# Optimization experiments

Measured on AMD Instinct MI355X. Metric: run time of the kernel, lower is better.

## Reference

```python
import jax, jax.numpy as jnp
import numpy as np
import math

FACIL_RATE = 2.0
FIRE_THRESH = 0.85
MAX_GATE = 8.0
N_BUF = 512
TOP_K_FRAC = 0.1
B, T, D = 4, 4096, 2048


def _gelu(x):
    c = math.sqrt(2.0 / math.pi)
    return 0.5 * x * (1.0 + jnp.tanh(c * (x + 0.044715 * x * x * x)))


def setup_inputs() -> dict:
    key = jax.random.key(0)
    k1, k2, k3 = jax.random.split(key, 3)
    x = jax.random.normal(k1, (B, T, D), dtype=jnp.float32)
    log_strength = jnp.asarray(0.0, dtype=jnp.float32)
    # Steady-state ring buffer: keys = normalized mean vectors, masks = top-k(|mean|) indicators
    means = jax.random.normal(k2, (N_BUF, D), dtype=jnp.float32)
    buf_keys = means / jnp.linalg.norm(means, axis=-1, keepdims=True)
    top_k = max(1, int(D * TOP_K_FRAC))  # 204
    _, top_idx = jax.lax.top_k(jnp.abs(means), top_k)  # (N_BUF, top_k)
    buf_masks = jnp.zeros((N_BUF, D), dtype=jnp.float32).at[
        jnp.arange(N_BUF)[:, None], top_idx].set(1.0)
    facil = 1.0 + 3.0 * jax.random.uniform(k3, (N_BUF,), dtype=jnp.float32)
    valid_mask = jnp.ones((N_BUF,), dtype=bool)
    return {"x": x, "log_strength": log_strength, "buf_keys": buf_keys,
            "buf_masks": buf_masks, "facil": facil, "valid_mask": valid_mask}


def reference(x, log_strength, buf_keys, buf_masks, facil, valid_mask):
    # Steady-state (pass1_complete) path of GELU277.forward
    y = _gelu(x)  # (B, T, D)
    # m_curr = y.detach().flatten(0,1).mean(0)  -> stop_gradient as in torch no_grad
    m_curr = jax.lax.stop_gradient(y).reshape(-1, y.shape[-1]).mean(0)  # (D,)
    q = m_curr / jnp.linalg.norm(m_curr)
    sims = buf_keys @ q                      # (N_BUF,) cosine similarities
    sims = jnp.where(valid_mask, sims, -1.0)
    nearest = jnp.argmax(sims)
    sim_max = sims[nearest]
    # facil[nearest] *= FACIL_RATE if fired, then read (.item() in torch -> constant)
    f = jax.lax.stop_gradient(facil[nearest]) * jnp.where(sim_max > FIRE_THRESH, FACIL_RATE, 1.0)
    # strength.item() in torch -> no grad through log_strength
    strength = jax.lax.stop_gradient(jnp.clip(jnp.exp(log_strength), 0.01, 5.0))
    k_amp = jnp.minimum(1.0 + strength * (f - 1.0), MAX_GATE)
    topk_mask = jax.lax.stop_gradient(buf_masks[nearest])  # (D,)
    gate = 1.0 + (k_amp - 1.0) * topk_mask
    return y * gate[None, None, :]
```

## Files before the change

### kernel.cpp

```cpp
#include <hip/hip_runtime.h>
#include <math.h>

#define DCOLS 2048
#define NROWS 16384
#define NBUF  512

typedef float v4f __attribute__((ext_vector_type(4)));

__device__ __forceinline__ float gelu_f(float x) {
    const float c = 0.7978845608028654f;
    float u = c * (x + 0.044715f * x * x * x);
    float e = __expf(2.0f * u);
    float t = 1.0f - 2.0f / (1.0f + e);
    return 0.5f * x * (1.0f + t);
}

__global__ __launch_bounds__(512) void k_colsum_part(const float* __restrict__ x,
                                                     float* __restrict__ part) {
    int t = threadIdx.x;
    int col = t * 4;
    float a0 = 0.f, a1 = 0.f, a2 = 0.f, a3 = 0.f;
    for (int r = blockIdx.x; r < NROWS; r += gridDim.x) {
        float4 v = *reinterpret_cast<const float4*>(x + (size_t)r * DCOLS + col);
        a0 += gelu_f(v.x); a1 += gelu_f(v.y); a2 += gelu_f(v.z); a3 += gelu_f(v.w);
    }
    float4 st; st.x = a0; st.y = a1; st.z = a2; st.w = a3;
    *reinterpret_cast<float4*>(part + (size_t)blockIdx.x * DCOLS + col) = st;
}

__global__ __launch_bounds__(512) void k_colsum_atomic(const float* __restrict__ x,
                                                       float* __restrict__ colsum) {
    int t = threadIdx.x;
    int col = t * 4;
    float a0 = 0.f, a1 = 0.f, a2 = 0.f, a3 = 0.f;
    for (int r = blockIdx.x; r < NROWS; r += gridDim.x) {
        float4 v = *reinterpret_cast<const float4*>(x + (size_t)r * DCOLS + col);
        a0 += gelu_f(v.x); a1 += gelu_f(v.y); a2 += gelu_f(v.z); a3 += gelu_f(v.w);
    }
    atomicAdd(&colsum[col + 0], a0);
    atomicAdd(&colsum[col + 1], a1);
    atomicAdd(&colsum[col + 2], a2);
    atomicAdd(&colsum[col + 3], a3);
}

__global__ __launch_bounds__(256) void k_colsum_reduce(const float* __restrict__ part,
                                                       float* __restrict__ colsum) {
    int col = blockIdx.x * 256 + threadIdx.x;
    int base = blockIdx.y * 64;
    float a = 0.f;
#pragma unroll 8
    for (int b = 0; b < 64; ++b)
        a += part[(size_t)(base + b) * DCOLS + col];
    atomicAdd(&colsum[col], a);
}

__global__ __launch_bounds__(256) void k_sims(const float* __restrict__ keys,
                                              const float* __restrict__ colsum,
                                              float* __restrict__ s) {
    __shared__ float wsum[4];
    int row = blockIdx.x;
    int t = threadIdx.x;
    const float* kr = keys + (size_t)row * DCOLS;
    int j = t * 8;
    float4 k0 = *reinterpret_cast<const float4*>(kr + j);
    float4 k1 = *reinterpret_cast<const float4*>(kr + j + 4);
    float4 c0 = *reinterpret_cast<const float4*>(colsum + j);
    float4 c1 = *reinterpret_cast<const float4*>(colsum + j + 4);
    float acc = k0.x * c0.x + k0.y * c0.y + k0.z * c0.z + k0.w * c0.w
              + k1.x * c1.x + k1.y * c1.y + k1.z * c1.z + k1.w * c1.w;
    for (int off = 32; off; off >>= 1) acc += __shfl_down(acc, off);
    if ((t & 63) == 0) wsum[t >> 6] = acc;
    __syncthreads();
    if (t == 0) s[row] = wsum[0] + wsum[1] + wsum[2] + wsum[3];
}

__global__ __launch_bounds__(256) void k_gate(const float* __restrict__ colsum,
                                              const float* __restrict__ s,
                                              const float* __restrict__ log_strength,
                                              const float* __restrict__ facil,
                                              const float* __restrict__ masks,
                                              float* __restrict__ gate) {
    __shared__ float red[256];
    __shared__ int   redi[256];
    int t = threadIdx.x;

    float n2 = 0.f;
    for (int j = t; j < DCOLS; j += 256) { float v = colsum[j]; n2 += v * v; }
    red[t] = n2; __syncthreads();
    for (int off = 128; off; off >>= 1) {
        if (t < off) red[t] += red[t + off];
        __syncthreads();
    }
    float norm = sqrtf(red[0]);
    __syncthreads();

    float best = -1e30f; int bi = 0x7fffffff;
    for (int j = t; j < NBUF; j += 256) {
        float v = s[j];
        if (v > best || (v == best && j < bi)) { best = v; bi = j; }
    }
    red[t] = best; redi[t] = bi; __syncthreads();
    for (int off = 128; off; off >>= 1) {
        if (t < off) {
            float ov = red[t + off]; int oi = redi[t + off];
            if (ov > red[t] || (ov == red[t] && oi < redi[t])) { red[t] = ov; redi[t] = oi; }
        }
        __syncthreads();
    }
    int nearest = redi[0];
    float sim_max = red[0] / norm;

    float strength = __expf(log_strength[0]);
    strength = fminf(fmaxf(strength, 0.01f), 5.0f);
    float f = facil[nearest] * (sim_max > 0.85f ? 2.0f : 1.0f);
    float k_amp = fminf(1.0f + strength * (f - 1.0f), 8.0f);

    const float* mrow = masks + (size_t)nearest * DCOLS;
    for (int j = t; j < DCOLS; j += 256)
        gate[j] = 1.0f + (k_amp - 1.0f) * mrow[j];
}

__global__ __launch_bounds__(256) void k_scale(const float* __restrict__ x,
                                               const float* __restrict__ gate,
                                               float* __restrict__ out) {
    int t = threadIdx.x;
    int col = t * 8;
    float4 g0 = *reinterpret_cast<const float4*>(gate + col);
    float4 g1 = *reinterpret_cast<const float4*>(gate + col + 4);
    for (int r = blockIdx.x; r < NROWS; r += gridDim.x) {
        size_t off = (size_t)r * DCOLS + col;
        float4 v0 = *reinterpret_cast<const float4*>(x + off);
        float4 v1 = *reinterpret_cast<const float4*>(x + off + 4);
        v4f o0, o1;
        o0.x = gelu_f(v0.x) * g0.x;
        o0.y = gelu_f(v0.y) * g0.y;
        o0.z = gelu_f(v0.z) * g0.z;
        o0.w = gelu_f(v0.w) * g0.w;
        o1.x = gelu_f(v1.x) * g1.x;
        o1.y = gelu_f(v1.y) * g1.y;
        o1.z = gelu_f(v1.z) * g1.z;
        o1.w = gelu_f(v1.w) * g1.w;
        __builtin_nontemporal_store(o0, reinterpret_cast<v4f*>(out + off));
        __builtin_nontemporal_store(o1, reinterpret_cast<v4f*>(out + off + 4));
    }
}

extern "C" void kernel_launch(void* const* d_in, const int* in_sizes, int n_in,
                              void* d_out, int out_size, void* d_ws, size_t ws_size,
                              hipStream_t stream) {
    const float* x            = (const float*)d_in[0];
    const float* log_strength = (const float*)d_in[1];
    const float* keys         = (const float*)d_in[2];
    const float* masks        = (const float*)d_in[3];
    const float* facil        = (const float*)d_in[4];
    float* out = (float*)d_out;
    float* ws  = (float*)d_ws;

    float* colsum = ws;
    float* s      = ws + 2048;
    float* gate   = ws + 2560;
    float* part   = ws + 4608;

    auto need = [](int nbp) {
        return (size_t)(4608 + (size_t)nbp * DCOLS) * sizeof(float);
    };

    int nbp = 0;
    if (ws_size >= need(1024)) nbp = 1024;
    else if (ws_size >= need(512)) nbp = 512;

    (void)hipMemsetAsync(colsum, 0, DCOLS * sizeof(float), stream);

    if (nbp) {
        k_colsum_part<<<nbp, 512, 0, stream>>>(x, part);
        dim3 rg(DCOLS / 256, nbp / 64);
        k_colsum_reduce<<<rg, 256, 0, stream>>>(part, colsum);
    } else {
        k_colsum_atomic<<<512, 512, 0, stream>>>(x, colsum);
    }
    k_sims<<<NBUF, 256, 0, stream>>>(keys, colsum, s);
    k_gate<<<1, 256, 0, stream>>>(colsum, s, log_strength, facil, masks, gate);
    k_scale<<<2048, 256, 0, stream>>>(x, gate, out);
}
```

Measured before the change: 95.41 us.

## Write GELU output in reduction pass and rescale only gated columns afterward

The first pass now writes GELU(x) straight to the output while it accumulates column sums, so the second pass no longer re-reads x or recomputes GELU. Instead a sparse pass reads back and rescales only the 8-column groups whose gate differs from 1. The similarity and gate kernels are merged through a last-block atomic counter, and the memset is folded into the first kernel, which removes launches. The risk is that about 57% of column groups hold a masked column, so the rescale pass may still touch most cache lines and add read-modify-write traffic.

```diff
diff --git a/kernel.cpp b/kernel.cpp
--- a/kernel.cpp
+++ b/kernel.cpp
@@ -15,32 +15,38 @@
     return 0.5f * x * (1.0f + t);
 }
 
-__global__ __launch_bounds__(512) void k_colsum_part(const float* __restrict__ x,
-                                                     float* __restrict__ part) {
+__global__ __launch_bounds__(512) void k_pass1(const float* __restrict__ x,
+                                               float* __restrict__ out,
+                                               float* __restrict__ part,
+                                               float* __restrict__ colsum,
+                                               int* __restrict__ counter,
+                                               int do_zero) {
     int t = threadIdx.x;
     int col = t * 4;
+    if (do_zero && blockIdx.x == 0) {
+        colsum[t] = 0.f; colsum[t + 512] = 0.f;
+        colsum[t + 1024] = 0.f; colsum[t + 1536] = 0.f;
+        if (t == 0) *counter = 0;
+    }
     float a0 = 0.f, a1 = 0.f, a2 = 0.f, a3 = 0.f;
+#pragma unroll 2
     for (int r = blockIdx.x; r < NROWS; r += gridDim.x) {
-        float4 v = *reinterpret_cast<const float4*>(x + (size_t)r * DCOLS + col);
-        a0 += gelu_f(v.x); a1 += gelu_f(v.y); a2 += gelu_f(v.z); a3 += gelu_f(v.w);
+        size_t off = (size_t)r * DCOLS + col;
+        v4f v = __builtin_nontemporal_load(reinterpret_cast<const v4f*>(x + off));
+        v4f o;
+        o.x = gelu_f(v.x); o.y = gelu_f(v.y); o.z = gelu_f(v.z); o.w = gelu_f(v.w);
+        a0 += o.x; a1 += o.y; a2 += o.z; a3 += o.w;
+        *reinterpret_cast<v4f*>(out + off) = o;
     }
-    float4 st; st.x = a0; st.y = a1; st.z = a2; st.w = a3;
-    *reinterpret_cast<float4*>(part + (size_t)blockIdx.x * DCOLS + col) = st;
-}
-
-__global__ __launch_bounds__(512) void k_colsum_atomic(const float* __restrict__ x,
-                                                       float* __restrict__ colsum) {
-    int t = threadIdx.x;
-    int col = t * 4;
-    float a0 = 0.f, a1 = 0.f, a2 = 0.f, a3 = 0.f;
-    for (int r = blockIdx.x; r < NROWS; r += gridDim.x) {
-        float4 v = *reinterpret_cast<const float4*>(x + (size_t)r * DCOLS + col);
-        a0 += gelu_f(v.x); a1 += gelu_f(v.y); a2 += gelu_f(v.z); a3 += gelu_f(v.w);
+    if (part) {
+        v4f st; st.x = a0; st.y = a1; st.z = a2; st.w = a3;
+        *reinterpret_cast<v4f*>(part + (size_t)blockIdx.x * DCOLS + col) = st;
+    } else {
+        atomicAdd(&colsum[col + 0], a0);
+        atomicAdd(&colsum[col + 1], a1);
+        atomicAdd(&colsum[col + 2], a2);
+        atomicAdd(&colsum[col + 3], a3);
     }
-    atomicAdd(&colsum[col + 0], a0);
-    atomicAdd(&colsum[col + 1], a1);
-    atomicAdd(&colsum[col + 2], a2);
-    atomicAdd(&colsum[col + 3], a3);
 }
 
 __global__ __launch_bounds__(256) void k_colsum_reduce(const float* __restrict__ part,
@@ -54,12 +60,20 @@
     atomicAdd(&colsum[col], a);
 }
 
-__global__ __launch_bounds__(256) void k_sims(const float* __restrict__ keys,
-                                              const float* __restrict__ colsum,
-                                              float* __restrict__ s) {
-    __shared__ float wsum[4];
+__global__ __launch_bounds__(256) void k_sims_gate(const float* __restrict__ keys,
+                                                   const float* __restrict__ colsum,
+                                                   float* __restrict__ s,
+                                                   const float* __restrict__ log_strength,
+                                                   const float* __restrict__ facil,
+                                                   const float* __restrict__ masks,
+                                                   float* __restrict__ gate,
+                                                   int* __restrict__ counter) {
+    __shared__ float red[256];
+    __shared__ int   redi[256];
+    __shared__ bool  last;
     int row = blockIdx.x;
     int t = threadIdx.x;
+
     const float* kr = keys + (size_t)row * DCOLS;
     int j = t * 8;
     float4 k0 = *reinterpret_cast<const float4*>(kr + j);
@@ -69,23 +83,20 @@
     float acc = k0.x * c0.x + k0.y * c0.y + k0.z * c0.z + k0.w * c0.w
               + k1.x * c1.x + k1.y * c1.y + k1.z * c1.z + k1.w * c1.w;
     for (int off = 32; off; off >>= 1) acc += __shfl_down(acc, off);
-    if ((t & 63) == 0) wsum[t >> 6] = acc;
+    if ((t & 63) == 0) red[t >> 6] = acc;
     __syncthreads();
-    if (t == 0) s[row] = wsum[0] + wsum[1] + wsum[2] + wsum[3];
-}
-
-__global__ __launch_bounds__(256) void k_gate(const float* __restrict__ colsum,
-                                              const float* __restrict__ s,
-                                              const float* __restrict__ log_strength,
-                                              const float* __restrict__ facil,
-                                              const float* __restrict__ masks,
-                                              float* __restrict__ gate) {
-    __shared__ float red[256];
-    __shared__ int   redi[256];
-    int t = threadIdx.x;
+    if (t == 0) {
+        s[row] = red[0] + red[1] + red[2] + red[3];
+        __threadfence();
+        int old = atomicAdd(counter, 1);
+        last = (old == (int)gridDim.x - 1);
+    }
+    __syncthreads();
+    if (!last) return;
+    __threadfence();
 
     float n2 = 0.f;
-    for (int j = t; j < DCOLS; j += 256) { float v = colsum[j]; n2 += v * v; }
+    for (int k = t; k < DCOLS; k += 256) { float v = colsum[k]; n2 += v * v; }
     red[t] = n2; __syncthreads();
     for (int off = 128; off; off >>= 1) {
         if (t < off) red[t] += red[t + off];
@@ -95,9 +106,9 @@
     __syncthreads();
 
     float best = -1e30f; int bi = 0x7fffffff;
-    for (int j = t; j < NBUF; j += 256) {
-        float v = s[j];
-        if (v > best || (v == best && j < bi)) { best = v; bi = j; }
+    for (int k = t; k < NBUF; k += 256) {
+        float v = s[k];
+        if (v > best || (v == best && k < bi)) { best = v; bi = k; }
     }
     red[t] = best; redi[t] = bi; __syncthreads();
     for (int off = 128; off; off >>= 1) {
@@ -116,32 +127,31 @@
     float k_amp = fminf(1.0f + strength * (f - 1.0f), 8.0f);
 
     const float* mrow = masks + (size_t)nearest * DCOLS;
-    for (int j = t; j < DCOLS; j += 256)
-        gate[j] = 1.0f + (k_amp - 1.0f) * mrow[j];
+    for (int k = t; k < DCOLS; k += 256)
+        gate[k] = 1.0f + (k_amp - 1.0f) * mrow[k];
 }
 
-__global__ __launch_bounds__(256) void k_scale(const float* __restrict__ x,
-                                               const float* __restrict__ gate,
-                                               float* __restrict__ out) {
+__global__ __launch_bounds__(256) void k_scale_sparse(float* __restrict__ out,
+                                                      const float* __restrict__ gate) {
     int t = threadIdx.x;
     int col = t * 8;
     float4 g0 = *reinterpret_cast<const float4*>(gate + col);
     float4 g1 = *reinterpret_cast<const float4*>(gate + col + 4);
+    bool a0 = (g0.x != 1.f) | (g0.y != 1.f) | (g0.z != 1.f) | (g0.w != 1.f);
+    bool a1 = (g1.x != 1.f) | (g1.y != 1.f) | (g1.z != 1.f) | (g1.w != 1.f);
+    if (!a0 && !a1) return;
     for (int r = blockIdx.x; r < NROWS; r += gridDim.x) {
         size_t off = (size_t)r * DCOLS + col;
-        float4 v0 = *reinterpret_cast<const float4*>(x + off);
-        float4 v1 = *reinterpret_cast<const float4*>(x + off + 4);
-        v4f o0, o1;
-        o0.x = gelu_f(v0.x) * g0.x;
-        o0.y = gelu_f(v0.y) * g0.y;
-        o0.z = gelu_f(v0.z) * g0.z;
-        o0.w = gelu_f(v0.w) * g0.w;
-        o1.x = gelu_f(v1.x) * g1.x;
-        o1.y = gelu_f(v1.y) * g1.y;
-        o1.z = gelu_f(v1.z) * g1.z;
-        o1.w = gelu_f(v1.w) * g1.w;
-        __builtin_nontemporal_store(o0, reinterpret_cast<v4f*>(out + off));
-        __builtin_nontemporal_store(o1, reinterpret_cast<v4f*>(out + off + 4));
+        if (a0) {
+            float4 v = *reinterpret_cast<const float4*>(out + off);
+            v.x *= g0.x; v.y *= g0.y; v.z *= g0.z; v.w *= g0.w;
+            *reinterpret_cast<float4*>(out + off) = v;
+        }
+        if (a1) {
+            float4 v = *reinterpret_cast<const float4*>(out + off + 4);
+            v.x *= g1.x; v.y *= g1.y; v.z *= g1.z; v.w *= g1.w;
+            *reinterpret_cast<float4*>(out + off + 4) = v;
+        }
     }
 }
 
@@ -159,26 +169,26 @@
     float* colsum = ws;
     float* s      = ws + 2048;
     float* gate   = ws + 2560;
-    float* part   = ws + 4608;
+    int*   counter = (int*)(ws + 4608);
+    float* part   = ws + 4864;
 
     auto need = [](int nbp) {
-        return (size_t)(4608 + (size_t)nbp * DCOLS) * sizeof(float);
+        return (size_t)(4864 + (size_t)nbp * DCOLS) * sizeof(float);
     };
 
     int nbp = 0;
     if (ws_size >= need(1024)) nbp = 1024;
     else if (ws_size >= need(512)) nbp = 512;
 
-    (void)hipMemsetAsync(colsum, 0, DCOLS * sizeof(float), stream);
-
     if (nbp) {
-        k_colsum_part<<<nbp, 512, 0, stream>>>(x, part);
+        k_pass1<<<nbp, 512, 0, stream>>>(x, out, part, colsum, counter, 1);
         dim3 rg(DCOLS / 256, nbp / 64);
         k_colsum_reduce<<<rg, 256, 0, stream>>>(part, colsum);
     } else {
-        k_colsum_atomic<<<512, 512, 0, stream>>>(x, colsum);
+        (void)hipMemsetAsync(ws, 0, 4864 * sizeof(float), stream);
+        k_pass1<<<512, 512, 0, stream>>>(x, out, nullptr, colsum, counter, 0);
     }
-    k_sims<<<NBUF, 256, 0, stream>>>(keys, colsum, s);
-    k_gate<<<1, 256, 0, stream>>>(colsum, s, log_strength, facil, masks, gate);
-    k_scale<<<2048, 256, 0, stream>>>(x, gate, out);
+    k_sims_gate<<<NBUF, 256, 0, stream>>>(keys, colsum, s, log_strength,
+                                          facil, masks, gate, counter);
+    k_scale_sparse<<<2048, 256, 0, stream>>>(out, gate);
 }
```

After: 114.1 us. +19.6%, slower.

## Fuse sims and gate via last-block counter, drop memset and atomics

Applied to the files above, without the earlier changes.

Merges the similarity and gate kernels into one launch, where the last block to finish (found through an atomic counter plus thread fences) computes the norm, argmax and gate. The counter is reset inside the partial-sum kernel, so the memset is no longer needed. The column-sum reduction becomes a single-pass, atomic-free LDS tree reduction over 512 partials, replacing the previous 1024. Together these cut two launches and the atomic traffic, at the cost of relying on a grid-wide last-block pattern and a shorter partial-sum grid.

```diff
diff --git a/kernel.cpp b/kernel.cpp
--- a/kernel.cpp
+++ b/kernel.cpp
@@ -4,6 +4,7 @@
 #define DCOLS 2048
 #define NROWS 16384
 #define NBUF  512
+#define NBP   512
 
 typedef float v4f __attribute__((ext_vector_type(4)));
 
@@ -15,12 +16,15 @@
     return 0.5f * x * (1.0f + t);
 }
 
-__global__ __launch_bounds__(512) void k_colsum_part(const float* __restrict__ x,
-                                                     float* __restrict__ part) {
+__global__ __launch_bounds__(512) void k_part(const float* __restrict__ x,
+                                              float* __restrict__ part,
+                                              int* __restrict__ cnt) {
     int t = threadIdx.x;
     int col = t * 4;
+    if (blockIdx.x == 0 && t == 0) *cnt = 0;
     float a0 = 0.f, a1 = 0.f, a2 = 0.f, a3 = 0.f;
-    for (int r = blockIdx.x; r < NROWS; r += gridDim.x) {
+#pragma unroll 2
+    for (int r = blockIdx.x; r < NROWS; r += NBP) {
         float4 v = *reinterpret_cast<const float4*>(x + (size_t)r * DCOLS + col);
         a0 += gelu_f(v.x); a1 += gelu_f(v.y); a2 += gelu_f(v.z); a3 += gelu_f(v.w);
     }
@@ -28,36 +32,44 @@
     *reinterpret_cast<float4*>(part + (size_t)blockIdx.x * DCOLS + col) = st;
 }
 
-__global__ __launch_bounds__(512) void k_colsum_atomic(const float* __restrict__ x,
-                                                       float* __restrict__ colsum) {
-    int t = threadIdx.x;
-    int col = t * 4;
-    float a0 = 0.f, a1 = 0.f, a2 = 0.f, a3 = 0.f;
-    for (int r = blockIdx.x; r < NROWS; r += gridDim.x) {
-        float4 v = *reinterpret_cast<const float4*>(x + (size_t)r * DCOLS + col);
-        a0 += gelu_f(v.x); a1 += gelu_f(v.y); a2 += gelu_f(v.z); a3 += gelu_f(v.w);
+__global__ __launch_bounds__(256) void k_reduce(const float* __restrict__ part,
+                                                float* __restrict__ colsum) {
+    __shared__ float4 lds[64][4];
+    int t  = threadIdx.x;
+    int tx = t & 3;
+    int ty = t >> 2;
+    int c  = blockIdx.x * 16 + tx * 4;
+    float4 acc = {0.f, 0.f, 0.f, 0.f};
+    for (int i = ty; i < NBP; i += 64) {
+        float4 p = *reinterpret_cast<const float4*>(part + (size_t)i * DCOLS + c);
+        acc.x += p.x; acc.y += p.y; acc.z += p.z; acc.w += p.w;
     }
-    atomicAdd(&colsum[col + 0], a0);
-    atomicAdd(&colsum[col + 1], a1);
-    atomicAdd(&colsum[col + 2], a2);
-    atomicAdd(&colsum[col + 3], a3);
+    lds[ty][tx] = acc;
+    __syncthreads();
+    for (int off = 32; off; off >>= 1) {
+        if (ty < off) {
+            float4 o = lds[ty + off][tx];
+            float4 m = lds[ty][tx];
+            m.x += o.x; m.y += o.y; m.z += o.z; m.w += o.w;
+            lds[ty][tx] = m;
+        }
+        __syncthreads();
+    }
+    if (ty == 0)
+        *reinterpret_cast<float4*>(colsum + c) = lds[0][tx];
 }
 
-__global__ __launch_bounds__(256) void k_colsum_reduce(const float* __restrict__ part,
-                                                       float* __restrict__ colsum) {
-    int col = blockIdx.x * 256 + threadIdx.x;
-    int base = blockIdx.y * 64;
-    float a = 0.f;
-#pragma unroll 8
-    for (int b = 0; b < 64; ++b)
-        a += part[(size_t)(base + b) * DCOLS + col];
-    atomicAdd(&colsum[col], a);
-}
-
-__global__ __launch_bounds__(256) void k_sims(const float* __restrict__ keys,
-                                              const float* __restrict__ colsum,
-                                              float* __restrict__ s) {
-    __shared__ float wsum[4];
+__global__ __launch_bounds__(256) void k_sims_gate(const float* __restrict__ keys,
+                                                   const float* __restrict__ colsum,
+                                                   float* __restrict__ s,
+                                                   const float* __restrict__ log_strength,
+                                                   const float* __restrict__ facil,
+                                                   const float* __restrict__ masks,
+                                                   float* __restrict__ gate,
+                                                   int* __restrict__ counter) {
+    __shared__ float red[256];
+    __shared__ int   redi[256];
+    __shared__ bool  last;
     int row = blockIdx.x;
     int t = threadIdx.x;
     const float* kr = keys + (size_t)row * DCOLS;
@@ -66,26 +78,22 @@
     float4 k1 = *reinterpret_cast<const float4*>(kr + j + 4);
     float4 c0 = *reinterpret_cast<const float4*>(colsum + j);
     float4 c1 = *reinterpret_cast<const float4*>(colsum + j + 4);
-    float acc = k0.x * c0.x + k0.y * c0.y + k0.z * c0.z + k0.w * c0.w
-              + k1.x * c1.x + k1.y * c1.y + k1.z * c1.z + k1.w * c1.w;
+    float acc = k0.x*c0.x + k0.y*c0.y + k0.z*c0.z + k0.w*c0.w
+              + k1.x*c1.x + k1.y*c1.y + k1.z*c1.z + k1.w*c1.w;
     for (int off = 32; off; off >>= 1) acc += __shfl_down(acc, off);
-    if ((t & 63) == 0) wsum[t >> 6] = acc;
+    if ((t & 63) == 0) red[t >> 6] = acc;
     __syncthreads();
-    if (t == 0) s[row] = wsum[0] + wsum[1] + wsum[2] + wsum[3];
-}
-
-__global__ __launch_bounds__(256) void k_gate(const float* __restrict__ colsum,
-                                              const float* __restrict__ s,
-                                              const float* __restrict__ log_strength,
-                                              const float* __restrict__ facil,
-                                              const float* __restrict__ masks,
-                                              float* __restrict__ gate) {
-    __shared__ float red[256];
-    __shared__ int   redi[256];
-    int t = threadIdx.x;
+    if (t == 0) {
+        s[row] = red[0] + red[1] + red[2] + red[3];
+        __threadfence();
+        last = (atomicAdd(counter, 1) == (int)gridDim.x - 1);
+    }
+    __syncthreads();
+    if (!last) return;
+    __threadfence();
 
     float n2 = 0.f;
-    for (int j = t; j < DCOLS; j += 256) { float v = colsum[j]; n2 += v * v; }
+    for (int k = t; k < DCOLS; k += 256) { float v = colsum[k]; n2 += v * v; }
     red[t] = n2; __syncthreads();
     for (int off = 128; off; off >>= 1) {
         if (t < off) red[t] += red[t + off];
@@ -95,9 +103,9 @@
     __syncthreads();
 
     float best = -1e30f; int bi = 0x7fffffff;
-    for (int j = t; j < NBUF; j += 256) {
-        float v = s[j];
-        if (v > best || (v == best && j < bi)) { best = v; bi = j; }
+    for (int k = t; k < NBUF; k += 256) {
+        float v = s[k];
+        if (v > best || (v == best && k < bi)) { best = v; bi = k; }
     }
     red[t] = best; redi[t] = bi; __syncthreads();
     for (int off = 128; off; off >>= 1) {
@@ -116,8 +124,8 @@
     float k_amp = fminf(1.0f + strength * (f - 1.0f), 8.0f);
 
     const float* mrow = masks + (size_t)nearest * DCOLS;
-    for (int j = t; j < DCOLS; j += 256)
-        gate[j] = 1.0f + (k_amp - 1.0f) * mrow[j];
+    for (int k = t; k < DCOLS; k += 256)
+        gate[k] = 1.0f + (k_amp - 1.0f) * mrow[k];
 }
 
 __global__ __launch_bounds__(256) void k_scale(const float* __restrict__ x,
@@ -132,17 +140,28 @@
         float4 v0 = *reinterpret_cast<const float4*>(x + off);
         float4 v1 = *reinterpret_cast<const float4*>(x + off + 4);
         v4f o0, o1;
-        o0.x = gelu_f(v0.x) * g0.x;
-        o0.y = gelu_f(v0.y) * g0.y;
-        o0.z = gelu_f(v0.z) * g0.z;
-        o0.w = gelu_f(v0.w) * g0.w;
-        o1.x = gelu_f(v1.x) * g1.x;
-        o1.y = gelu_f(v1.y) * g1.y;
-        o1.z = gelu_f(v1.z) * g1.z;
-        o1.w = gelu_f(v1.w) * g1.w;
+        o0.x = gelu_f(v0.x) * g0.x; o0.y = gelu_f(v0.y) * g0.y;
+        o0.z = gelu_f(v0.z) * g0.z; o0.w = gelu_f(v0.w) * g0.w;
+        o1.x = gelu_f(v1.x) * g1.x; o1.y = gelu_f(v1.y) * g1.y;
+        o1.z = gelu_f(v1.z) * g1.z; o1.w = gelu_f(v1.w) * g1.w;
         __builtin_nontemporal_store(o0, reinterpret_cast<v4f*>(out + off));
         __builtin_nontemporal_store(o1, reinterpret_cast<v4f*>(out + off + 4));
     }
+}
+
+__global__ __launch_bounds__(512) void k_colsum_atomic(const float* __restrict__ x,
+                                                       float* __restrict__ colsum) {
+    int t = threadIdx.x;
+    int col = t * 4;
+    float a0 = 0.f, a1 = 0.f, a2 = 0.f, a3 = 0.f;
+    for (int r = blockIdx.x; r < NROWS; r += gridDim.x) {
+        float4 v = *reinterpret_cast<const float4*>(x + (size_t)r * DCOLS + col);
+        a0 += gelu_f(v.x); a1 += gelu_f(v.y); a2 += gelu_f(v.z); a3 += gelu_f(v.w);
+    }
+    atomicAdd(&colsum[col + 0], a0);
+    atomicAdd(&colsum[col + 1], a1);
+    atomicAdd(&colsum[col + 2], a2);
+    atomicAdd(&colsum[col + 3], a3);
 }
 
 extern "C" void kernel_launch(void* const* d_in, const int* in_sizes, int n_in,
@@ -159,26 +178,19 @@
     float* colsum = ws;
     float* s      = ws + 2048;
     float* gate   = ws + 2560;
-    float* part   = ws + 4608;
+    int*   cnt    = (int*)(ws + 4608);
+    float* part   = ws + 4864;
 
-    auto need = [](int nbp) {
-        return (size_t)(4608 + (size_t)nbp * DCOLS) * sizeof(float);
-    };
+    size_t need = (size_t)(4864 + (size_t)NBP * DCOLS) * sizeof(float);
 
-    int nbp = 0;
-    if (ws_size >= need(1024)) nbp = 1024;
-    else if (ws_size >= need(512)) nbp = 512;
-
-    (void)hipMemsetAsync(colsum, 0, DCOLS * sizeof(float), stream);
-
-    if (nbp) {
-        k_colsum_part<<<nbp, 512, 0, stream>>>(x, part);
-        dim3 rg(DCOLS / 256, nbp / 64);
-        k_colsum_reduce<<<rg, 256, 0, stream>>>(part, colsum);
+    if (ws_size >= need) {
+        k_part<<<NBP, 512, 0, stream>>>(x, part, cnt);
+        k_reduce<<<DCOLS / 16, 256, 0, stream>>>(part, colsum);
     } else {
+        (void)hipMemsetAsync(ws, 0, 4864 * sizeof(float), stream);
         k_colsum_atomic<<<512, 512, 0, stream>>>(x, colsum);
     }
-    k_sims<<<NBUF, 256, 0, stream>>>(keys, colsum, s);
-    k_gate<<<1, 256, 0, stream>>>(colsum, s, log_strength, facil, masks, gate);
+    k_sims_gate<<<NBUF, 256, 0, stream>>>(keys, colsum, s, log_strength,
+                                          facil, masks, gate, cnt);
     k_scale<<<2048, 256, 0, stream>>>(x, gate, out);
 }
```

Result: slower. 100.9 us (+5.7%).
